# Performance work log

Measured on AMD Instinct MI355X. Metric: run time of the kernel, lower is better.

## Reference

```python
import jax, jax.numpy as jnp
import numpy as np

N_NODES = 100000
N_EDGES = 3200000
N_GRAPHS = 512


def setup_inputs() -> dict:
    key = jax.random.key(0)
    k1, k2, k3, k4, k5 = jax.random.split(key, 5)
    x = jax.random.normal(k1, (N_NODES, 5), dtype=jnp.float32)
    edge_index = jax.random.randint(k2, (2, N_EDGES), 0, N_NODES, dtype=jnp.int64)
    batch = jnp.sort(jax.random.randint(k3, (N_NODES,), 0, N_GRAPHS, dtype=jnp.int64))
    W1 = jax.random.normal(k4, (5, 16), dtype=jnp.float32) * (1.0 / np.sqrt(5.0))
    b1 = jnp.zeros((16,), dtype=jnp.float32)
    W2 = jax.random.normal(k5, (16, 16), dtype=jnp.float32) * 0.25
    b2 = jnp.zeros((16,), dtype=jnp.float32)
    return {"x": x, "edge_index": edge_index, "batch": batch,
            "W1": W1, "b1": b1, "W2": W2, "b2": b2}


def _gcn_conv(x, src, dst, norm, W, b, n_nodes):
    # PyG GCNConv: h = X W; out_i = sum_{j->i} norm_ij * h_j + b
    h = x @ W                                   # [N, out]
    msgs = h[src] * norm[:, None]               # gather + scale  [E_tot, out]
    out = jax.ops.segment_sum(msgs, dst, num_segments=n_nodes)
    return out + b


def reference(x, edge_index, batch, W1, b1, W2, b2):
    n = x.shape[0]
    # add self-loops (GCNConv default)
    loops = jnp.arange(n, dtype=edge_index.dtype)
    src = jnp.concatenate([edge_index[0], loops])
    dst = jnp.concatenate([edge_index[1], loops])
    # symmetric normalization: deg computed on destination nodes
    deg = jax.ops.segment_sum(jnp.ones_like(src, dtype=x.dtype), dst, num_segments=n)
    dinv = jnp.where(deg > 0, jax.lax.rsqrt(deg), 0.0)
    norm = dinv[src] * dinv[dst]                # [E_tot]

    h = jax.nn.relu(_gcn_conv(x, src, dst, norm, W1, b1, n))
    h = jax.nn.relu(_gcn_conv(h, src, dst, norm, W2, b2, n))

    # global mean pool over graphs in the batch
    sums = jax.ops.segment_sum(h, batch, num_segments=N_GRAPHS)
    cnts = jax.ops.segment_sum(jnp.ones((n,), dtype=h.dtype), batch, num_segments=N_GRAPHS)
    return sums / jnp.maximum(cnts, 1.0)[:, None]
```

## Files before the change

kernel.cpp:

```cpp
#include <hip/hip_runtime.h>

#define N_NODES  100000
#define N_EDGES  3200000
#define N_GRAPHS 512
#define F_IN     5
#define F_HID    16

#define PBLK   512
#define CHUNK  4096
#define NBLK   ((N_EDGES + CHUNK - 1) / CHUNK)
#define BKT_NODES 256
#define NBKT ((N_NODES + BKT_NODES - 1) / BKT_NODES)
#define HPAD   512
#define CAP    10240
#define CPT    (CAP / 512)
#define PN     64
#define NPB    ((N_NODES + PN - 1) / PN)


__device__ inline unsigned short f2bf(float f) {
    unsigned u = __float_as_uint(f);
    return (unsigned short)((u + 0x7fffu + ((u >> 16) & 1u)) >> 16);
}
__device__ inline float bf2f(unsigned short h) {
    return __uint_as_float(((unsigned)h) << 16);
}
__device__ inline void unpack16(uint4 r0, uint4 r1, float* f) {
    f[0]  = bf2f((unsigned short)r0.x); f[1]  = bf2f((unsigned short)(r0.x >> 16));
    f[2]  = bf2f((unsigned short)r0.y); f[3]  = bf2f((unsigned short)(r0.y >> 16));
    f[4]  = bf2f((unsigned short)r0.z); f[5]  = bf2f((unsigned short)(r0.z >> 16));
    f[6]  = bf2f((unsigned short)r0.w); f[7]  = bf2f((unsigned short)(r0.w >> 16));
    f[8]  = bf2f((unsigned short)r1.x); f[9]  = bf2f((unsigned short)(r1.x >> 16));
    f[10] = bf2f((unsigned short)r1.y); f[11] = bf2f((unsigned short)(r1.y >> 16));
    f[12] = bf2f((unsigned short)r1.z); f[13] = bf2f((unsigned short)(r1.z >> 16));
    f[14] = bf2f((unsigned short)r1.w); f[15] = bf2f((unsigned short)(r1.w >> 16));
}

template <int NW>
__device__ inline int block_incl_scan(int v, int t, int* wsum) {
    int lane = t & 63, wave = t >> 6;
    int x = v;
#pragma unroll
    for (int o = 1; o < 64; o <<= 1) {
        int y = __shfl_up(x, o, 64);
        if (lane >= o) x += y;
    }
    if (lane == 63) wsum[wave] = x;
    __syncthreads();
    if (t < 64) {
        int w = (t < NW) ? wsum[t] : 0;
#pragma unroll
        for (int o = 1; o < NW; o <<= 1) {
            int y = __shfl_up(w, o, 64);
            if (t >= o) w += y;
        }
        if (t < NW) wsum[t] = w;
    }
    __syncthreads();
    return x + (wave ? wsum[wave - 1] : 0);
}


__global__ __launch_bounds__(256) void k_zero(float* __restrict__ out,
                                              float* __restrict__ cnt) {
    int i = blockIdx.x * 256 + threadIdx.x;
    if (i < N_GRAPHS * F_HID) out[i] = 0.0f;
    if (i < N_GRAPHS) cnt[i] = 0.0f;
}

__global__ __launch_bounds__(PBLK) void k_count(const int* __restrict__ dst,
                                                const int* __restrict__ batch,
                                                int* __restrict__ H,
                                                int* __restrict__ Hc,
                                                unsigned short* __restrict__ rnk_e,
                                                float* __restrict__ cnt) {
    __shared__ int hist[HPAD];
    __shared__ int bcnt[8];
    __shared__ int g0s;
    int t = threadIdx.x, blk = blockIdx.x;
    int chunk0 = blk * CHUNK;
    int n4 = min(CHUNK, N_EDGES - chunk0) >> 2;
    hist[t] = 0;
    if (t < 8) bcnt[t] = 0;
    if (t == 0 && blk < NBKT) {
        int nb = blk * BKT_NODES;
        g0s = batch[nb < N_NODES ? nb : N_NODES - 1];
    }
    __syncthreads();
    const int4* d4 = (const int4*)(dst + chunk0);
    ushort4* r4 = (ushort4*)(rnk_e + chunk0);
#pragma unroll
    for (int i = 0; i < CHUNK / 4 / PBLK; i++) {
        int k = t + i * PBLK;
        if (k < n4) {
            int4 d = d4[k];
            ushort4 rr;
            rr.x = (unsigned short)atomicAdd(&hist[d.x >> 8], 1);
            rr.y = (unsigned short)atomicAdd(&hist[d.y >> 8], 1);
            rr.z = (unsigned short)atomicAdd(&hist[d.z >> 8], 1);
            rr.w = (unsigned short)atomicAdd(&hist[d.w >> 8], 1);
            r4[k] = rr;
        }
    }
    if (blk < NBKT && t < BKT_NODES) {
        int i2 = blk * BKT_NODES + t;
        if (i2 < N_NODES) {
            int g = batch[i2];
            int l = g - g0s;
            if (l >= 0 && l < 8) atomicAdd(&bcnt[l], 1);
            else atomicAdd(&cnt[g], 1.0f);
        }
    }
    __syncthreads();
    int v = hist[t];
    H[blk * HPAD + t] = v;
    Hc[blk * HPAD + t] = v;
    if (blk < NBKT && t < 8 && bcnt[t] > 0) atomicAdd(&cnt[g0s + t], (float)bcnt[t]);
}

__global__ __launch_bounds__(256) void k_scan(int* __restrict__ H,
                                              int* __restrict__ cnt_b) {
    __shared__ int wsum[8];
    int b = blockIdx.x, t = threadIdx.x;
    int v[4];
    int s = 0;
#pragma unroll
    for (int i = 0; i < 4; i++) {
        int pos = t * 4 + i;
        v[i] = (pos < NBLK) ? H[pos * HPAD + b] : 0;
        s += v[i];
    }
    int incl = block_incl_scan<4>(s, t, wsum);
    int run = incl - s;
#pragma unroll
    for (int i = 0; i < 4; i++) {
        int pos = t * 4 + i;
        if (pos < NBLK) H[pos * HPAD + b] = run;
        run += v[i];
    }
    if (t == 255) cnt_b[b] = incl;
}

__global__ __launch_bounds__(PBLK) void k_scatter(const int* __restrict__ src,
                                                  const int* __restrict__ dst,
                                                  const int* __restrict__ H,
                                                  const int* __restrict__ Hc,
                                                  const unsigned short* __restrict__ rnk_e,
                                                  unsigned* __restrict__ packed) {
    __shared__ int scn[HPAD];
    __shared__ int base[HPAD];
    __shared__ int wsum[8];
    __shared__ unsigned pkd[CHUNK];
    __shared__ unsigned short bkt[CHUNK];
    int t = threadIdx.x, blk = blockIdx.x;
    int chunk0 = blk * CHUNK;
    int n = min(CHUNK, N_EDGES - chunk0);
    int n4 = n >> 2;
    base[t] = H[blk * HPAD + t];
    int v = Hc[blk * HPAD + t];
    int incl = block_incl_scan<8>(v, t, wsum);
    scn[t] = incl - v;
    __syncthreads();
    const int4* s4 = (const int4*)(src + chunk0);
    const int4* d4 = (const int4*)(dst + chunk0);
    const ushort4* r4 = (const ushort4*)(rnk_e + chunk0);
#pragma unroll
    for (int i = 0; i < CHUNK / 4 / PBLK; i++) {
        int k = t + i * PBLK;
        if (k < n4) {
            int4 s = s4[k], d = d4[k];
            ushort4 r = r4[k];
            int b0 = d.x >> 8, b1 = d.y >> 8, b2 = d.z >> 8, b3 = d.w >> 8;
            int p0 = scn[b0] + r.x;
            pkd[p0] = ((unsigned)s.x << 8) | (unsigned)(d.x & 255);
            bkt[p0] = (unsigned short)b0;
            int p1 = scn[b1] + r.y;
            pkd[p1] = ((unsigned)s.y << 8) | (unsigned)(d.y & 255);
            bkt[p1] = (unsigned short)b1;
            int p2 = scn[b2] + r.z;
            pkd[p2] = ((unsigned)s.z << 8) | (unsigned)(d.z & 255);
            bkt[p2] = (unsigned short)b2;
            int p3 = scn[b3] + r.w;
            pkd[p3] = ((unsigned)s.w << 8) | (unsigned)(d.w & 255);
            bkt[p3] = (unsigned short)b3;
        }
    }
    __syncthreads();
    for (int p = t; p < n; p += PBLK) {
        int b = bkt[p];
        packed[(size_t)b * CAP + base[b] + (p - scn[b])] = pkd[p];
    }
}

__global__ __launch_bounds__(512) void k_csr(const int* __restrict__ cnt_b,
                                             const unsigned* __restrict__ packed,
                                             const float* __restrict__ x,
                                             const float* __restrict__ W1,
                                             int2* __restrict__ rowbc,
                                             int* __restrict__ col,
                                             float* __restrict__ dinv,
                                             unsigned short* __restrict__ pb) {
    __shared__ int hist[BKT_NODES];
    __shared__ int beg[BKT_NODES];
    __shared__ int wsum[8];
    __shared__ float w1[F_IN * F_HID];
    __shared__ unsigned pkd[CAP];
    __shared__ int tots;
    int b = blockIdx.x, t = threadIdx.x;
    int gbase = b * CAP;
    if (t < BKT_NODES) hist[t] = 0;
    if (t == 0) tots = min(cnt_b[b], CAP);
    if (t >= 512 - F_IN * F_HID) w1[t - (512 - F_IN * F_HID)] = W1[t - (512 - F_IN * F_HID)];
    __syncthreads();
    int tot = tots;
    const unsigned* pk = packed + (size_t)b * CAP;
    int r2[CPT];
#pragma unroll
    for (int i = 0; i < CPT; i++) {
        int k = t + i * 512;
        if (k < tot) {
            unsigned u = pk[k];
            pkd[k] = u;
            r2[i] = atomicAdd(&hist[u & 255], 1);
        }
    }
    __syncthreads();
    int v = (t < BKT_NODES) ? hist[t] : 0;
    int incl = block_incl_scan<8>(v, t, wsum);
    if (t < BKT_NODES) beg[t] = incl - v;
    __syncthreads();
#pragma unroll
    for (int i = 0; i < CPT; i++) {
        int k = t + i * 512;
        if (k < tot) {
            unsigned w = pkd[k];
            col[gbase + beg[w & 255] + r2[i]] = (int)(w >> 8);
        }
    }
    if (t < BKT_NODES) {
        int node = b * BKT_NODES + t;
        if (node < N_NODES) {
            rowbc[node] = make_int2(gbase + beg[t], v);
            float di = rsqrtf((float)(1 + v));
            dinv[node] = di;
            float xi[F_IN];
#pragma unroll
            for (int k = 0; k < F_IN; k++) xi[k] = x[node * F_IN + k];
            unsigned pkk[8];
#pragma unroll
            for (int q = 0; q < 8; q++) {
                float h0 = 0.0f, h1 = 0.0f;
#pragma unroll
                for (int k = 0; k < F_IN; k++) {
                    h0 += xi[k] * w1[k * F_HID + 2 * q];
                    h1 += xi[k] * w1[k * F_HID + 2 * q + 1];
                }
                pkk[q] = (unsigned)f2bf(h0 * di) | ((unsigned)f2bf(h1 * di) << 16);
            }
            uint4* d4 = (uint4*)(pb + (size_t)node * F_HID);
            d4[0] = make_uint4(pkk[0], pkk[1], pkk[2], pkk[3]);
            d4[1] = make_uint4(pkk[4], pkk[5], pkk[6], pkk[7]);
        }
    }
}

__global__ __launch_bounds__(256) void k_pull1(const int2* __restrict__ rowbc,
                                               const int* __restrict__ col,
                                               const unsigned short* __restrict__ pb,
                                               const float* __restrict__ dinv,
                                               const float* __restrict__ W2,
                                               const float* __restrict__ b1,
                                               unsigned short* __restrict__ pb2) {
    __shared__ float w2[F_HID * F_HID];
    __shared__ float b1s[F_HID];
    int t = threadIdx.x;
    w2[t] = W2[t];
    if (t < F_HID) b1s[t] = b1[t];
    __syncthreads();
    int nl = t >> 2, q = t & 3;
    int node = blockIdx.x * PN + nl;
    const uint4* pb16 = (const uint4*)pb;
    float f[F_HID];
#pragma unroll
    for (int c = 0; c < F_HID; c++) f[c] = 0.0f;
    if (node < N_NODES) {
        int2 rc = rowbc[node];
        if (q == 0) unpack16(pb16[2 * node], pb16[2 * node + 1], f);
        for (int i = q; i < rc.y; i += 4) {
            int s = col[rc.x + i];
            uint4 r0 = pb16[2 * s], r1 = pb16[2 * s + 1];
            float g[F_HID];
            unpack16(r0, r1, g);
#pragma unroll
            for (int c = 0; c < F_HID; c++) f[c] += g[c];
        }
    }
#pragma unroll
    for (int c = 0; c < F_HID; c++) {
        f[c] += __shfl_xor(f[c], 1, 64);
        f[c] += __shfl_xor(f[c], 2, 64);
    }
    if (node < N_NODES) {
        float di = dinv[node];
        float h[F_HID];
#pragma unroll
        for (int c = 0; c < F_HID; c++)
            h[c] = fmaxf(di * f[c] + b1s[c], 0.0f);
        float m0 = 0.0f, m1 = 0.0f, m2 = 0.0f, m3 = 0.0f;
#pragma unroll
        for (int c = 0; c < F_HID; c++) {
            float4 wv = *(const float4*)&w2[c * F_HID + 4 * q];
            m0 += h[c] * wv.x; m1 += h[c] * wv.y; m2 += h[c] * wv.z; m3 += h[c] * wv.w;
        }
        unsigned p0 = (unsigned)f2bf(m0 * di) | ((unsigned)f2bf(m1 * di) << 16);
        unsigned p1 = (unsigned)f2bf(m2 * di) | ((unsigned)f2bf(m3 * di) << 16);
        *(uint2*)(pb2 + (size_t)node * F_HID + 4 * q) = make_uint2(p0, p1);
    }
}

__global__ __launch_bounds__(256) void k_pull2(const int2* __restrict__ rowbc,
                                               const int* __restrict__ col,
                                               const unsigned short* __restrict__ pb,
                                               const float* __restrict__ dinv,
                                               const int* __restrict__ batch,
                                               const float* __restrict__ b2,
                                               const float* __restrict__ cnt,
                                               float* __restrict__ out) {
    __shared__ float b2s[F_HID];
    __shared__ float hbuf[PN][F_HID + 1];
    __shared__ int bl[PN];
    int t = threadIdx.x;
    if (t < F_HID) b2s[t] = b2[t];
    if (t < PN) {
        int nn = blockIdx.x * PN + t;
        bl[t] = (nn < N_NODES) ? batch[nn] : -1;
    }
    __syncthreads();
    int nl = t >> 2, q = t & 3;
    int node = blockIdx.x * PN + nl;
    const uint4* pb16 = (const uint4*)pb;
    float f[F_HID];
#pragma unroll
    for (int c = 0; c < F_HID; c++) f[c] = 0.0f;
    if (node < N_NODES) {
        int2 rc = rowbc[node];
        if (q == 0) unpack16(pb16[2 * node], pb16[2 * node + 1], f);
        for (int i = q; i < rc.y; i += 4) {
            int s = col[rc.x + i];
            uint4 r0 = pb16[2 * s], r1 = pb16[2 * s + 1];
            float g[F_HID];
            unpack16(r0, r1, g);
#pragma unroll
            for (int c = 0; c < F_HID; c++) f[c] += g[c];
        }
    }
#pragma unroll
    for (int c = 0; c < F_HID; c++) {
        f[c] += __shfl_xor(f[c], 1, 64);
        f[c] += __shfl_xor(f[c], 2, 64);
    }
    if (node < N_NODES && q == 0) {
        float di = dinv[node];
#pragma unroll
        for (int c = 0; c < F_HID; c++)
            hbuf[nl][c] = fmaxf(di * f[c] + b2s[c], 0.0f);
    }
    __syncthreads();
    if (t < 8 * F_HID) {
        int l = t >> 4, ch = t & 15;
        int g = bl[0] + l;
        if (g < N_GRAPHS) {
            float s = 0.0f;
            int m = 0;
            for (int n0 = 0; n0 < PN; n0++) {
                int n = (n0 + (ch << 2)) & (PN - 1);
                if (bl[n] == g) { s += hbuf[n][ch]; m++; }
            }
            if (m > 0) atomicAdd(&out[g * F_HID + ch], s / cnt[g]);
        }
    }
}


extern "C" void kernel_launch(void* const* d_in, const int* in_sizes, int n_in,
                              void* d_out, int out_size, void* d_ws, size_t ws_size,
                              hipStream_t stream) {
    const float* x     = (const float*)d_in[0];
    const int*   ei    = (const int*)d_in[1];
    const int*   batch = (const int*)d_in[2];
    const float* W1    = (const float*)d_in[3];
    const float* b1    = (const float*)d_in[4];
    const float* W2    = (const float*)d_in[5];
    const float* b2    = (const float*)d_in[6];
    float* out = (float*)d_out;

    int*            H      = (int*)d_ws;
    int*            Hc     = H + (size_t)NBLK * HPAD;
    int*            cnt_b  = Hc + (size_t)NBLK * HPAD;
    unsigned short* rnk_e  = (unsigned short*)(cnt_b + 512);
    unsigned*       packed = (unsigned*)(rnk_e + (size_t)N_EDGES);
    int2*           rowbc  = (int2*)(packed + (size_t)NBKT * CAP);
    int*            col    = (int*)(rowbc + N_NODES);
    float*          dinv   = (float*)(col + (size_t)NBKT * CAP);
    unsigned short* pb_a   = (unsigned short*)(dinv + N_NODES);
    unsigned short* pb_b   = pb_a + (size_t)N_NODES * F_HID;
    float*          cnt    = (float*)(pb_b + (size_t)N_NODES * F_HID);

    const int* src = ei;
    const int* dst = ei + N_EDGES;

    k_zero   <<<(N_GRAPHS * F_HID + 255) / 256, 256, 0, stream>>>(out, cnt);
    k_count  <<<NBLK, PBLK, 0, stream>>>(dst, batch, H, Hc, rnk_e, cnt);
    k_scan   <<<NBKT, 256, 0, stream>>>(H, cnt_b);
    k_scatter<<<NBLK, PBLK, 0, stream>>>(src, dst, H, Hc, rnk_e, packed);
    k_csr    <<<NBKT, 512, 0, stream>>>(cnt_b, packed, x, W1, rowbc, col, dinv, pb_a);
    k_pull1  <<<NPB, 256, 0, stream>>>(rowbc, col, pb_a, dinv, W2, b1, pb_b);
    k_pull2  <<<NPB, 256, 0, stream>>>(rowbc, col, pb_b, dinv, batch, b2, cnt, out);
}
```

Measured before the change: 197.8 us.

## Fuse all GCN pipeline stages into one cooperative persistent kernel with grid syncs

```diff
diff --git a/kernel.cpp b/kernel.cpp
--- a/kernel.cpp
+++ b/kernel.cpp
@@ -1,4 +1,7 @@
 #include <hip/hip_runtime.h>
+#include <hip/hip_cooperative_groups.h>
+
+namespace cg = cooperative_groups;
 
 #define N_NODES  100000
 #define N_EDGES  3200000
@@ -16,6 +19,9 @@
 #define CPT    (CAP / 512)
 #define PN     64
 #define NPB    ((N_NODES + PN - 1) / PN)
+#define GRID_F 512
+#define PNF    128
+#define NPGF   ((N_NODES + PNF - 1) / PNF)
 
 
 __device__ inline unsigned short f2bf(float f) {
@@ -58,6 +64,307 @@
     }
     __syncthreads();
     return x + (wave ? wsum[wave - 1] : 0);
+}
+
+
+union SMF {
+    struct { int hist[HPAD]; } cnt;
+    struct { int scn[HPAD]; int base[HPAD];
+             unsigned pkd[CHUNK]; unsigned short bkt[CHUNK]; } sc;
+    struct { int hist[BKT_NODES]; int beg[BKT_NODES];
+             float w1[F_IN * F_HID]; unsigned pkd[CAP]; } csr;
+    struct { float w2[F_HID * F_HID]; float b1s[F_HID]; } p1;
+    struct { float b2s[F_HID]; float hbuf[PNF][F_HID + 1]; int bl[PNF]; } p2;
+};
+
+__global__ __launch_bounds__(512, 2) void k_fused(
+        const float* __restrict__ x, const int* __restrict__ ei,
+        const int* __restrict__ batch, const float* __restrict__ W1,
+        const float* __restrict__ b1, const float* __restrict__ W2,
+        const float* __restrict__ b2, float* __restrict__ out,
+        int* __restrict__ H, int* __restrict__ Hc, int* __restrict__ cnt_b,
+        unsigned short* __restrict__ rnk_e, unsigned* __restrict__ packed,
+        int2* __restrict__ rowbc, int* __restrict__ col,
+        float* __restrict__ dinv, unsigned short* __restrict__ pb_a,
+        unsigned short* __restrict__ pb_b, float* __restrict__ cnt) {
+    cg::grid_group grid = cg::this_grid();
+    const int* src = ei;
+    const int* dst = ei + N_EDGES;
+    int t = threadIdx.x, bid = blockIdx.x;
+    static __shared__ SMF sm;
+    __shared__ int wsum[8];
+    __shared__ int bcnt[8];
+    __shared__ int g0s, tots;
+
+    {
+        int i = bid * 512 + t;
+        if (i < N_GRAPHS * F_HID) out[i] = 0.0f;
+        if (i < N_GRAPHS) cnt[i] = 0.0f;
+    }
+    grid.sync();
+
+    for (int blk = bid; blk < NBLK; blk += GRID_F) {
+        int chunk0 = blk * CHUNK;
+        int n4 = min(CHUNK, N_EDGES - chunk0) >> 2;
+        sm.cnt.hist[t] = 0;
+        __syncthreads();
+        const int4* d4 = (const int4*)(dst + chunk0);
+        ushort4* r4 = (ushort4*)(rnk_e + chunk0);
+#pragma unroll
+        for (int i = 0; i < CHUNK / 4 / PBLK; i++) {
+            int k = t + i * PBLK;
+            if (k < n4) {
+                int4 d = d4[k];
+                ushort4 rr;
+                rr.x = (unsigned short)atomicAdd(&sm.cnt.hist[d.x >> 8], 1);
+                rr.y = (unsigned short)atomicAdd(&sm.cnt.hist[d.y >> 8], 1);
+                rr.z = (unsigned short)atomicAdd(&sm.cnt.hist[d.z >> 8], 1);
+                rr.w = (unsigned short)atomicAdd(&sm.cnt.hist[d.w >> 8], 1);
+                r4[k] = rr;
+            }
+        }
+        __syncthreads();
+        int v = sm.cnt.hist[t];
+        H[blk * HPAD + t] = v;
+        Hc[blk * HPAD + t] = v;
+        __syncthreads();
+    }
+    grid.sync();
+
+    for (int b = bid; b < NBKT; b += GRID_F) {
+        int v[2];
+        int s = 0;
+#pragma unroll
+        for (int i = 0; i < 2; i++) {
+            int pos = t * 2 + i;
+            v[i] = (pos < NBLK) ? H[pos * HPAD + b] : 0;
+            s += v[i];
+        }
+        int incl = block_incl_scan<8>(s, t, wsum);
+        int run = incl - s;
+#pragma unroll
+        for (int i = 0; i < 2; i++) {
+            int pos = t * 2 + i;
+            if (pos < NBLK) H[pos * HPAD + b] = run;
+            run += v[i];
+        }
+        if (t == 511) cnt_b[b] = incl;
+        __syncthreads();
+    }
+    grid.sync();
+
+    for (int blk = bid; blk < NBLK; blk += GRID_F) {
+        int chunk0 = blk * CHUNK;
+        int n = min(CHUNK, N_EDGES - chunk0);
+        int n4 = n >> 2;
+        sm.sc.base[t] = H[blk * HPAD + t];
+        int v = Hc[blk * HPAD + t];
+        int incl = block_incl_scan<8>(v, t, wsum);
+        sm.sc.scn[t] = incl - v;
+        __syncthreads();
+        const int4* s4 = (const int4*)(src + chunk0);
+        const int4* d4 = (const int4*)(dst + chunk0);
+        const ushort4* r4 = (const ushort4*)(rnk_e + chunk0);
+#pragma unroll
+        for (int i = 0; i < CHUNK / 4 / PBLK; i++) {
+            int k = t + i * PBLK;
+            if (k < n4) {
+                int4 s = s4[k], d = d4[k];
+                ushort4 r = r4[k];
+                int b0 = d.x >> 8, b1_ = d.y >> 8, b2_ = d.z >> 8, b3 = d.w >> 8;
+                int p0 = sm.sc.scn[b0] + r.x;
+                sm.sc.pkd[p0] = ((unsigned)s.x << 8) | (unsigned)(d.x & 255);
+                sm.sc.bkt[p0] = (unsigned short)b0;
+                int p1 = sm.sc.scn[b1_] + r.y;
+                sm.sc.pkd[p1] = ((unsigned)s.y << 8) | (unsigned)(d.y & 255);
+                sm.sc.bkt[p1] = (unsigned short)b1_;
+                int p2 = sm.sc.scn[b2_] + r.z;
+                sm.sc.pkd[p2] = ((unsigned)s.z << 8) | (unsigned)(d.z & 255);
+                sm.sc.bkt[p2] = (unsigned short)b2_;
+                int p3 = sm.sc.scn[b3] + r.w;
+                sm.sc.pkd[p3] = ((unsigned)s.w << 8) | (unsigned)(d.w & 255);
+                sm.sc.bkt[p3] = (unsigned short)b3;
+            }
+        }
+        __syncthreads();
+        for (int p = t; p < n; p += PBLK) {
+            int b = sm.sc.bkt[p];
+            packed[(size_t)b * CAP + sm.sc.base[b] + (p - sm.sc.scn[b])] = sm.sc.pkd[p];
+        }
+        __syncthreads();
+    }
+    grid.sync();
+
+    for (int b = bid; b < NBKT; b += GRID_F) {
+        int gbase = b * CAP;
+        if (t < BKT_NODES) sm.csr.hist[t] = 0;
+        if (t < 8) bcnt[t] = 0;
+        if (t == 0) {
+            tots = min(cnt_b[b], CAP);
+            g0s = batch[b * BKT_NODES];
+        }
+        if (t >= 512 - F_IN * F_HID)
+            sm.csr.w1[t - (512 - F_IN * F_HID)] = W1[t - (512 - F_IN * F_HID)];
+        __syncthreads();
+        int tot = tots;
+        const unsigned* pk = packed + (size_t)b * CAP;
+        int r2[CPT];
+#pragma unroll
+        for (int i = 0; i < CPT; i++) {
+            int k = t + i * 512;
+            if (k < tot) {
+                unsigned u = pk[k];
+                sm.csr.pkd[k] = u;
+                r2[i] = atomicAdd(&sm.csr.hist[u & 255], 1);
+            }
+        }
+        __syncthreads();
+        int v = (t < BKT_NODES) ? sm.csr.hist[t] : 0;
+        int incl = block_incl_scan<8>(v, t, wsum);
+        if (t < BKT_NODES) sm.csr.beg[t] = incl - v;
+        __syncthreads();
+#pragma unroll
+        for (int i = 0; i < CPT; i++) {
+            int k = t + i * 512;
+            if (k < tot) {
+                unsigned w = sm.csr.pkd[k];
+                col[gbase + sm.csr.beg[w & 255] + r2[i]] = (int)(w >> 8);
+            }
+        }
+        if (t < BKT_NODES) {
+            int node = b * BKT_NODES + t;
+            if (node < N_NODES) {
+                rowbc[node] = make_int2(gbase + sm.csr.beg[t], v);
+                float di = rsqrtf((float)(1 + v));
+                dinv[node] = di;
+                int g = batch[node];
+                int l = g - g0s;
+                if (l >= 0 && l < 8) atomicAdd(&bcnt[l], 1);
+                else atomicAdd(&cnt[g], 1.0f);
+                float xi[F_IN];
+#pragma unroll
+                for (int k = 0; k < F_IN; k++) xi[k] = x[node * F_IN + k];
+                unsigned pkk[8];
+#pragma unroll
+                for (int q = 0; q < 8; q++) {
+                    float h0 = 0.0f, h1 = 0.0f;
+#pragma unroll
+                    for (int k = 0; k < F_IN; k++) {
+                        h0 += xi[k] * sm.csr.w1[k * F_HID + 2 * q];
+                        h1 += xi[k] * sm.csr.w1[k * F_HID + 2 * q + 1];
+                    }
+                    pkk[q] = (unsigned)f2bf(h0 * di) | ((unsigned)f2bf(h1 * di) << 16);
+                }
+                uint4* d4 = (uint4*)(pb_a + (size_t)node * F_HID);
+                d4[0] = make_uint4(pkk[0], pkk[1], pkk[2], pkk[3]);
+                d4[1] = make_uint4(pkk[4], pkk[5], pkk[6], pkk[7]);
+            }
+        }
+        __syncthreads();
+        if (t < 8 && bcnt[t] > 0) atomicAdd(&cnt[g0s + t], (float)bcnt[t]);
+        __syncthreads();
+    }
+    grid.sync();
+
+    if (t < F_HID * F_HID) sm.p1.w2[t] = W2[t];
+    if (t >= 256 && t < 256 + F_HID) sm.p1.b1s[t - 256] = b1[t - 256];
+    __syncthreads();
+    for (int gw = bid; gw < NPGF; gw += GRID_F) {
+        int nl = t >> 2, q = t & 3;
+        int node = gw * PNF + nl;
+        const uint4* pb16 = (const uint4*)pb_a;
+        float f[F_HID];
+#pragma unroll
+        for (int c = 0; c < F_HID; c++) f[c] = 0.0f;
+        if (node < N_NODES) {
+            int2 rc = rowbc[node];
+            if (q == 0) unpack16(pb16[2 * node], pb16[2 * node + 1], f);
+            for (int i = q; i < rc.y; i += 4) {
+                int s = col[rc.x + i];
+                uint4 r0 = pb16[2 * s], r1 = pb16[2 * s + 1];
+                float g[F_HID];
+                unpack16(r0, r1, g);
+#pragma unroll
+                for (int c = 0; c < F_HID; c++) f[c] += g[c];
+            }
+        }
+#pragma unroll
+        for (int c = 0; c < F_HID; c++) {
+            f[c] += __shfl_xor(f[c], 1, 64);
+            f[c] += __shfl_xor(f[c], 2, 64);
+        }
+        if (node < N_NODES) {
+            float di = dinv[node];
+            float h[F_HID];
+#pragma unroll
+            for (int c = 0; c < F_HID; c++)
+                h[c] = fmaxf(di * f[c] + sm.p1.b1s[c], 0.0f);
+            float m0 = 0.0f, m1 = 0.0f, m2 = 0.0f, m3 = 0.0f;
+#pragma unroll
+            for (int c = 0; c < F_HID; c++) {
+                float4 wv = *(const float4*)&sm.p1.w2[c * F_HID + 4 * q];
+                m0 += h[c] * wv.x; m1 += h[c] * wv.y;
+                m2 += h[c] * wv.z; m3 += h[c] * wv.w;
+            }
+            unsigned p0 = (unsigned)f2bf(m0 * di) | ((unsigned)f2bf(m1 * di) << 16);
+            unsigned p1 = (unsigned)f2bf(m2 * di) | ((unsigned)f2bf(m3 * di) << 16);
+            *(uint2*)(pb_b + (size_t)node * F_HID + 4 * q) = make_uint2(p0, p1);
+        }
+    }
+    grid.sync();
+
+    for (int gw = bid; gw < NPGF; gw += GRID_F) {
+        if (t < F_HID) sm.p2.b2s[t] = b2[t];
+        if (t < PNF) {
+            int nn = gw * PNF + t;
+            sm.p2.bl[t] = (nn < N_NODES) ? batch[nn] : -1;
+        }
+        __syncthreads();
+        int nl = t >> 2, q = t & 3;
+        int node = gw * PNF + nl;
+        const uint4* pb16 = (const uint4*)pb_b;
+        float f[F_HID];
+#pragma unroll
+        for (int c = 0; c < F_HID; c++) f[c] = 0.0f;
+        if (node < N_NODES) {
+            int2 rc = rowbc[node];
+            if (q == 0) unpack16(pb16[2 * node], pb16[2 * node + 1], f);
+            for (int i = q; i < rc.y; i += 4) {
+                int s = col[rc.x + i];
+                uint4 r0 = pb16[2 * s], r1 = pb16[2 * s + 1];
+                float g[F_HID];
+                unpack16(r0, r1, g);
+#pragma unroll
+                for (int c = 0; c < F_HID; c++) f[c] += g[c];
+            }
+        }
+#pragma unroll
+        for (int c = 0; c < F_HID; c++) {
+            f[c] += __shfl_xor(f[c], 1, 64);
+            f[c] += __shfl_xor(f[c], 2, 64);
+        }
+        if (node < N_NODES && q == 0) {
+            float di = dinv[node];
+#pragma unroll
+            for (int c = 0; c < F_HID; c++)
+                sm.p2.hbuf[nl][c] = fmaxf(di * f[c] + sm.p2.b2s[c], 0.0f);
+        }
+        __syncthreads();
+        if (t < 8 * F_HID) {
+            int l = t >> 4, ch = t & 15;
+            int g = sm.p2.bl[0] + l;
+            if (g < N_GRAPHS) {
+                float s = 0.0f;
+                int m = 0;
+                for (int n0 = 0; n0 < PNF; n0++) {
+                    int n = (n0 + (ch << 3)) & (PNF - 1);
+                    if (sm.p2.bl[n] == g) { s += sm.p2.hbuf[n][ch]; m++; }
+                }
+                if (m > 0) atomicAdd(&out[g * F_HID + ch], s / cnt[g]);
+            }
+        }
+        __syncthreads();
+    }
 }
 
 
@@ -82,10 +389,7 @@
     int n4 = min(CHUNK, N_EDGES - chunk0) >> 2;
     hist[t] = 0;
     if (t < 8) bcnt[t] = 0;
-    if (t == 0 && blk < NBKT) {
-        int nb = blk * BKT_NODES;
-        g0s = batch[nb < N_NODES ? nb : N_NODES - 1];
-    }
+    if (t == 0 && blk < NBKT) g0s = batch[blk * BKT_NODES];
     __syncthreads();
     const int4* d4 = (const int4*)(dst + chunk0);
     ushort4* r4 = (ushort4*)(rnk_e + chunk0);
@@ -409,11 +713,29 @@
     const int* src = ei;
     const int* dst = ei + N_EDGES;
 
-    k_zero   <<<(N_GRAPHS * F_HID + 255) / 256, 256, 0, stream>>>(out, cnt);
-    k_count  <<<NBLK, PBLK, 0, stream>>>(dst, batch, H, Hc, rnk_e, cnt);
-    k_scan   <<<NBKT, 256, 0, stream>>>(H, cnt_b);
-    k_scatter<<<NBLK, PBLK, 0, stream>>>(src, dst, H, Hc, rnk_e, packed);
-    k_csr    <<<NBKT, 512, 0, stream>>>(cnt_b, packed, x, W1, rowbc, col, dinv, pb_a);
-    k_pull1  <<<NPB, 256, 0, stream>>>(rowbc, col, pb_a, dinv, W2, b1, pb_b);
-    k_pull2  <<<NPB, 256, 0, stream>>>(rowbc, col, pb_b, dinv, batch, b2, cnt, out);
-}
+    const float* ax = x; const int* aei = ei; const int* abatch = batch;
+    const float* aW1 = W1; const float* ab1 = b1; const float* aW2 = W2;
+    const float* ab2 = b2; float* aout = out;
+    int* aH = H; int* aHc = Hc; int* acnt_b = cnt_b;
+    unsigned short* arnk_e = rnk_e; unsigned* apacked = packed;
+    int2* arowbc = rowbc; int* acol = col; float* adinv = dinv;
+    unsigned short* apb_a = pb_a; unsigned short* apb_b = pb_b; float* acnt = cnt;
+
+    void* args[] = {&ax, &aei, &abatch, &aW1, &ab1, &aW2, &ab2, &aout,
+                    &aH, &aHc, &acnt_b, &arnk_e, &apacked, &arowbc, &acol,
+                    &adinv, &apb_a, &apb_b, &acnt};
+
+    hipError_t err = hipLaunchCooperativeKernel((const void*)k_fused,
+                                                dim3(GRID_F), dim3(512),
+                                                args, 0, stream);
+    if (err != hipSuccess) {
+        (void)hipGetLastError();
+        k_zero   <<<(N_GRAPHS * F_HID + 255) / 256, 256, 0, stream>>>(out, cnt);
+        k_count  <<<NBLK, PBLK, 0, stream>>>(dst, batch, H, Hc, rnk_e, cnt);
+        k_scan   <<<NBKT, 256, 0, stream>>>(H, cnt_b);
+        k_scatter<<<NBLK, PBLK, 0, stream>>>(src, dst, H, Hc, rnk_e, packed);
+        k_csr    <<<NBKT, 512, 0, stream>>>(cnt_b, packed, x, W1, rowbc, col, dinv, pb_a);
+        k_pull1  <<<NPB, 256, 0, stream>>>(rowbc, col, pb_a, dinv, W2, b1, pb_b);
+        k_pull2  <<<NPB, 256, 0, stream>>>(rowbc, col, pb_b, dinv, batch, b2, cnt, out);
+    }
+}
```

New measurement: 591.0 us. 2.99x slower.
